# Performance work log

Measured on AMD Instinct MI355X. Metric: run time of the kernel, lower is better.

Reference implementation:

```python
import jax, jax.numpy as jnp
import numpy as np

N, IN_DIM, OUT_DIM, NUM_HOPS, SD = 8192, 256, 256, 4, 64
ETA, LAM_LAP, LAM_SP, EPS = 0.5, 0.3, 0.05, 0.5
LN_EPS = 1e-5


def setup_inputs() -> dict:
    key = jax.random.key(0)
    ks = jax.random.split(key, 6)
    K = NUM_HOPS + 1
    return {
        "H": jax.random.normal(ks[0], (N, IN_DIM), jnp.float32),
        "hops": jax.random.normal(ks[1], (K, N, IN_DIM), jnp.float32),
        "L": jax.random.normal(ks[2], (N, N), jnp.float32),
        "U": jax.random.normal(ks[3], (K, IN_DIM, SD), jnp.float32) * 0.1,
        "W_in": jax.random.normal(ks[4], (OUT_DIM, IN_DIM), jnp.float32) * 0.05,
        "ln_gamma": jnp.ones((OUT_DIM,), jnp.float32),
        "ln_beta": jnp.zeros((OUT_DIM,), jnp.float32),
        "log_tau": jnp.zeros((), jnp.float32),
    }


def _per_hop(U_k, H_k):
    n = H_k.shape[0]
    Q, _ = jnp.linalg.qr(U_k)                 # [in_dim, sd]
    Z = Q.T @ H_k.T                           # [sd, n]
    G = Z @ Z.T                               # [sd, sd] Gram, reused
    Sigma = G / (n + 1e-8)
    tr_S = jnp.trace(Sigma)
    tr_S2 = jnp.sum(Sigma * Sigma)            # trace(Sigma @ Sigma), Sigma symmetric
    rank_eff = tr_S ** 2 / (tr_S2 + 1e-8)
    coeff = SD / (n * EPS ** 2 + 1e-8)
    M = jnp.eye(SD, dtype=Z.dtype) + coeff * G
    Lc = jnp.linalg.cholesky(M)
    MiZ = jax.scipy.linalg.cho_solve((Lc, True), Z)  # [sd, n]
    grad_R = (Q @ MiZ).T                      # [n, in_dim]
    return rank_eff, grad_R


def reference(H, hops, L, U, W_in, ln_gamma, ln_beta, log_tau):
    tau = jnp.clip(jnp.exp(log_tau), 0.1, 10.0)
    rank_effs, grads_R = jax.vmap(_per_hop)(U, hops)      # [K], [K,n,in_dim]
    lap_terms = jnp.einsum('nm,kmd->knd', L, hops)        # [K,n,in_dim]
    w = jax.nn.softmax(rank_effs / tau)                   # [K]
    grad_sum = jnp.einsum('k,knd->nd', w, grads_R)
    lap_sum = jnp.einsum('k,knd->nd', w, lap_terms)
    H_half = H + ETA * grad_sum - ETA * LAM_LAP * lap_sum
    H_prox = jnp.sign(H_half) * jax.nn.relu(jnp.abs(H_half) - LAM_SP * ETA)
    H_out = H_prox @ W_in.T
    mu = jnp.mean(H_out, axis=-1, keepdims=True)
    var = jnp.var(H_out, axis=-1, keepdims=True)
    H_out = (H_out - mu) * jax.lax.rsqrt(var + LN_EPS) * ln_gamma + ln_beta
    return H_out, rank_effs, w
```

## Files before the change

### kernel.cpp

```cpp
#include <hip/hip_runtime.h>
#include <stdint.h>


typedef __attribute__((ext_vector_type(8))) short  s16x8;
typedef __attribute__((ext_vector_type(4))) float  f32x4;

#define NNODE 8192
#define DIN   256
#define KHOP  5
#define SDM   64

static const size_t OFF_Q    = 0;
static const size_t OFF_QT   = OFF_Q   + (size_t)5*256*64*4;
static const size_t OFF_ZT   = OFF_QT  + (size_t)5*64*256*2;
static const size_t OFF_GP   = OFF_ZT  + (size_t)5*8192*64*2;
static const size_t OFF_LM   = OFF_GP  + (size_t)5*16*4096*4;
static const size_t OFF_RD   = OFF_LM  + (size_t)5*4096*4;
static const size_t OFF_LU   = OFF_RD  + (size_t)5*64*4;
static const size_t OFF_RDU  = OFF_LU  + (size_t)5*4096*4;
static const size_t OFF_RE   = OFF_RDU + (size_t)5*64*4;
static const size_t OFF_W    = OFF_RE  + 64;
static const size_t OFF_T2   = OFF_W   + 64;
static const size_t OFF_HWT  = OFF_T2  + (size_t)5*256*64*2;
static const size_t OFF_WBF  = OFF_HWT + (size_t)256*8192*2;
static const size_t OFF_HP   = OFF_WBF + (size_t)256*256*2;
static const size_t OFF_PART = OFF_HP  + (size_t)8192*256*2;
static const size_t OFF_HPRE = OFF_PART;
static const size_t OFF_LBF  = OFF_PART + (size_t)9*8192*256*2;

__device__ __forceinline__ unsigned short f2bf(float f){
  unsigned u = __builtin_bit_cast(unsigned, f);
  u += 0x7FFFu + ((u >> 16) & 1u);
  return (unsigned short)(u >> 16);
}
__device__ __forceinline__ float bf2f(unsigned h){
  return __builtin_bit_cast(float, h << 16);
}
__device__ __forceinline__ void gl_lds16(const void* g, void* l){
  __builtin_amdgcn_global_load_lds(
      (const __attribute__((address_space(1))) void*)g,
      (__attribute__((address_space(3))) void*)l, 16, 0, 0);
}
__device__ __forceinline__ f32x4 mfma16(s16x8 a, s16x8 b, f32x4 c){
  return __builtin_amdgcn_mfma_f32_16x16x32_bf16(a, b, c, 0, 0, 0);
}

__device__ void chol64(float* A, float* rd, int tid){
  #pragma unroll 1
  for (int j = 0; j < 64; ++j){
    if (tid == 0){
      float d = sqrtf(fmaxf(A[j*65+j], 1e-20f));
      A[j*65+j] = d; rd[j] = 1.0f / d;
    }
    __syncthreads();
    float rinv = rd[j];
    for (int i = j+1+tid; i < 64; i += 256) A[i*65+j] *= rinv;
    __syncthreads();
    int rem = 63 - j;
    for (int e = tid; e < rem*rem; e += 256){
      int i = j+1 + e/rem;
      int l = j+1 + (e - (e/rem)*rem);
      if (l <= i) A[i*65+l] -= A[i*65+j] * A[l*65+j];
    }
    __syncthreads();
  }
}

__global__ __launch_bounds__(256) void k_lbf(const float* __restrict__ L,
                                             unsigned short* __restrict__ Lbf){
  size_t e = ((size_t)blockIdx.x*256 + threadIdx.x)*8;
  f32x4 a = *(const f32x4*)(L + e);
  f32x4 b = *(const f32x4*)(L + e + 4);
  uint4 u;
  u.x = (unsigned)f2bf(a[0]) | ((unsigned)f2bf(a[1]) << 16);
  u.y = (unsigned)f2bf(a[2]) | ((unsigned)f2bf(a[3]) << 16);
  u.z = (unsigned)f2bf(b[0]) | ((unsigned)f2bf(b[1]) << 16);
  u.w = (unsigned)f2bf(b[2]) | ((unsigned)f2bf(b[3]) << 16);
  *(uint4*)(Lbf + e) = u;
}

__global__ __launch_bounds__(256) void k_gramchol(const float* __restrict__ U,
                                                  float* __restrict__ Lu,
                                                  float* __restrict__ rdu){
  int k = blockIdx.x, tid = threadIdx.x;
  __shared__ float Ul[256*65];
  __shared__ float A[64*65];
  __shared__ float rd[64];
  const float* Uk = U + (size_t)k*16384;
  for (int e = tid; e < 16384; e += 256) Ul[(e>>6)*65 + (e&63)] = Uk[e];
  __syncthreads();
  int ti = tid >> 4, tj = tid & 15;
  float s[16];
  #pragma unroll
  for (int i = 0; i < 16; ++i) s[i] = 0.0f;
  for (int n = 0; n < 256; ++n){
    float xa[4], xb[4];
    #pragma unroll
    for (int p = 0; p < 4; ++p){ xa[p] = Ul[n*65 + ti*4 + p]; xb[p] = Ul[n*65 + tj*4 + p]; }
    #pragma unroll
    for (int p = 0; p < 4; ++p)
      #pragma unroll
      for (int q = 0; q < 4; ++q) s[p*4+q] += xa[p]*xb[q];
  }
  #pragma unroll
  for (int p = 0; p < 4; ++p)
    #pragma unroll
    for (int q = 0; q < 4; ++q) A[(ti*4+p)*65 + tj*4+q] = s[p*4+q];
  __syncthreads();
  chol64(A, rd, tid);
  for (int e = tid; e < 4096; e += 256) Lu[(size_t)k*4096 + e] = A[(e>>6)*65 + (e&63)];
  if (tid < 64) rdu[k*64 + tid] = rd[tid];
}

__global__ __launch_bounds__(256) void k_qsolve(const float* __restrict__ U,
                                                const float* __restrict__ Lu,
                                                const float* __restrict__ rdu,
                                                float* __restrict__ Qf,
                                                unsigned short* __restrict__ Qt){
  int k = blockIdx.y, tid = threadIdx.x, wave = tid >> 6, lane = tid & 63;
  __shared__ float Al[64*65];
  __shared__ float rds[64];
  for (int e = tid; e < 4096; e += 256) Al[(e>>6)*65 + (e&63)] = Lu[(size_t)k*4096 + e];
  if (tid < 64) rds[tid] = rdu[k*64 + tid];
  __syncthreads();
  int n = blockIdx.x*4 + wave;
  float x = U[((size_t)k*256 + n)*64 + lane];
  #pragma unroll
  for (int j = 0; j < 64; ++j){
    float zj = __shfl(x, j) * rds[j];
    x = (lane == j) ? zj : (lane > j ? x - Al[lane*65+j]*zj : x);
  }
  Qf[((size_t)k*256 + n)*64 + lane] = x;
  Qt[(size_t)k*16384 + lane*256 + n] = f2bf(x);
}

__global__ __launch_bounds__(256,2) void k_zgemm(const float* __restrict__ hops,
                                                 const unsigned short* __restrict__ Qt,
                                                 unsigned short* __restrict__ Zt){
  __shared__ __align__(16) unsigned short Al[128][72];
  __shared__ __align__(16) unsigned short Bl[64][64];
  int tid = threadIdx.x, lane = tid & 63, wave = tid >> 6;
  int q = lane >> 4, r = lane & 15;
  int k = blockIdx.y, m0 = blockIdx.x * 128;
  f32x4 acc[2][4];
  #pragma unroll
  for (int a = 0; a < 2; ++a)
    #pragma unroll
    for (int b = 0; b < 4; ++b) acc[a][b] = (f32x4){0,0,0,0};
  int rr = tid >> 1, half = tid & 1;
  for (int it = 0; it < 4; ++it){
    __syncthreads();
    #pragma unroll
    for (int i = 0; i < 2; ++i){
      int o = i*4096 + wave*1024 + lane*16;
      int srow = o >> 7, kc = (o & 127) >> 1;
      gl_lds16(Qt + (size_t)k*16384 + srow*256 + it*64 + kc,
               (char*)&Bl[0][0] + i*4096 + wave*1024);
    }
    const float* ga = hops + ((size_t)k*NNODE + m0 + rr)*256 + it*64 + half*32;
    f32x4 v[8];
    #pragma unroll
    for (int i = 0; i < 8; ++i) v[i] = *(const f32x4*)(ga + i*4);
    #pragma unroll
    for (int i = 0; i < 4; ++i){
      s16x8 t;
      #pragma unroll
      for (int j = 0; j < 8; ++j){ int e = i*8+j; t[j] = (short)f2bf(v[e>>2][e&3]); }
      *(s16x8*)&Al[rr][half*32 + i*8] = t;
    }
    __syncthreads();
    #pragma unroll
    for (int h = 0; h < 2; ++h){
      int ko = h*32 + q*8;
      s16x8 b[4];
      #pragma unroll
      for (int ni = 0; ni < 4; ++ni) b[ni] = *(const s16x8*)&Bl[ni*16 + r][ko];
      #pragma unroll
      for (int mi = 0; mi < 2; ++mi){
        s16x8 a = *(const s16x8*)&Al[wave*32 + mi*16 + r][ko];
        #pragma unroll
        for (int ni = 0; ni < 4; ++ni) acc[mi][ni] = mfma16(a, b[ni], acc[mi][ni]);
      }
    }
  }
  #pragma unroll
  for (int mi = 0; mi < 2; ++mi)
    #pragma unroll
    for (int ni = 0; ni < 4; ++ni)
      #pragma unroll
      for (int ii = 0; ii < 4; ++ii){
        int m = m0 + wave*32 + mi*16 + q*4 + ii;
        int sc = ni*16 + r;
        Zt[((size_t)k*NNODE + m)*64 + sc] = f2bf(acc[mi][ni][ii]);
      }
}

__global__ __launch_bounds__(256) void k_gpart(const unsigned short* __restrict__ Zt,
                                               float* __restrict__ Gp){
  int k = blockIdx.x, c = blockIdx.y, tid = threadIdx.x;
  __shared__ __align__(16) unsigned short Zl[128][64];
  int ti = tid >> 4, tj = tid & 15;
  float acc[16];
  #pragma unroll
  for (int i = 0; i < 16; ++i) acc[i] = 0.0f;
  for (int sub = 0; sub < 4; ++sub){
    const char* gb = (const char*)Zt + ((size_t)k*NNODE + c*512 + sub*128)*128;
    __syncthreads();
    #pragma unroll
    for (int i = 0; i < 4; ++i){
      int o = i*4096 + tid*16;
      *(uint4*)((char*)&Zl[0][0] + o) = *(const uint4*)(gb + o);
    }
    __syncthreads();
    for (int n = 0; n < 128; ++n){
      const unsigned short* row = &Zl[n][0];
      uint2 ua = *(const uint2*)(row + ti*4);
      uint2 ub = *(const uint2*)(row + tj*4);
      float xa[4] = { bf2f(ua.x & 0xffff), bf2f(ua.x >> 16), bf2f(ua.y & 0xffff), bf2f(ua.y >> 16) };
      float xb[4] = { bf2f(ub.x & 0xffff), bf2f(ub.x >> 16), bf2f(ub.y & 0xffff), bf2f(ub.y >> 16) };
      #pragma unroll
      for (int p = 0; p < 4; ++p)
        #pragma unroll
        for (int qn = 0; qn < 4; ++qn) acc[p*4+qn] += xa[p]*xb[qn];
    }
  }
  float* o = Gp + ((size_t)k*16 + c)*4096;
  #pragma unroll
  for (int p = 0; p < 4; ++p)
    #pragma unroll
    for (int qn = 0; qn < 4; ++qn) o[(ti*4+p)*64 + tj*4+qn] = acc[p*4+qn];
}

__global__ __launch_bounds__(256) void k_gred(const float* __restrict__ Gp,
                                              float* __restrict__ LmO,
                                              float* __restrict__ rdO,
                                              float* __restrict__ reO){
  int k = blockIdx.x, tid = threadIdx.x;
  __shared__ float A[64*65];
  __shared__ float rd[64];
  __shared__ float red[256];
  int ti = tid >> 4, tj = tid & 15;
  float s[16];
  #pragma unroll
  for (int i = 0; i < 16; ++i) s[i] = 0.0f;
  for (int c = 0; c < 16; ++c){
    const float* g = Gp + ((size_t)k*16 + c)*4096 + (ti*4)*64 + tj*4;
    #pragma unroll
    for (int p = 0; p < 4; ++p)
      #pragma unroll
      for (int qn = 0; qn < 4; ++qn) s[p*4+qn] += g[p*64+qn];
  }
  const float sc    = 1.0f / (8192.0f + 1e-8f);
  const float coeff = 64.0f / (8192.0f*0.25f + 1e-8f);
  float trp = 0.0f, tr2p = 0.0f;
  #pragma unroll
  for (int p = 0; p < 4; ++p)
    #pragma unroll
    for (int qn = 0; qn < 4; ++qn){
      float gg = s[p*4+qn];
      float sg = gg * sc;
      tr2p += sg*sg;
      int row = ti*4+p, col = tj*4+qn;
      if (row == col) trp += sg;
      A[row*65 + col] = (row == col ? 1.0f : 0.0f) + coeff*gg;
    }
  red[tid] = trp; __syncthreads();
  for (int o = 128; o > 0; o >>= 1){ if (tid < o) red[tid] += red[tid+o]; __syncthreads(); }
  float tr = red[0]; __syncthreads();
  red[tid] = tr2p; __syncthreads();
  for (int o = 128; o > 0; o >>= 1){ if (tid < o) red[tid] += red[tid+o]; __syncthreads(); }
  float tr2 = red[0]; __syncthreads();
  if (tid == 0) reO[k] = tr*tr / (tr2 + 1e-8f);
  chol64(A, rd, tid);
  for (int e = tid; e < 4096; e += 256) LmO[(size_t)k*4096 + e] = A[(e>>6)*65 + (e&63)];
  if (tid < 64) rdO[k*64 + tid] = rd[tid];
}

__global__ void k_soft(const float* __restrict__ re, const float* __restrict__ ltau,
                       float* __restrict__ wv, float* __restrict__ dtail){
  if (threadIdx.x == 0){
    float tau = expf(ltau[0]);
    tau = fminf(fmaxf(tau, 0.1f), 10.0f);
    float r[5], m = -1e30f;
    for (int i = 0; i < 5; ++i){ r[i] = re[i]; m = fmaxf(m, r[i]); }
    float e[5], sum = 0.0f;
    for (int i = 0; i < 5; ++i){ e[i] = expf((r[i]-m)/tau); sum += e[i]; }
    for (int i = 0; i < 5; ++i){
      float w = e[i]/sum;
      wv[i] = w; dtail[i] = r[i]; dtail[5+i] = w;
    }
  }
}

__global__ __launch_bounds__(256) void k_t2w(const float* __restrict__ Qf,
                                             const float* __restrict__ LmI,
                                             const float* __restrict__ rdI,
                                             const float* __restrict__ wv,
                                             unsigned short* __restrict__ T2w){
  int k = blockIdx.y, tid = threadIdx.x, wave = tid >> 6, lane = tid & 63;
  __shared__ float Al[64*65];
  __shared__ float rds[64];
  for (int e = tid; e < 4096; e += 256) Al[(e>>6)*65 + (e&63)] = LmI[(size_t)k*4096 + e];
  if (tid < 64) rds[tid] = rdI[k*64 + tid];
  __syncthreads();
  int n = blockIdx.x*4 + wave;
  float x = Qf[((size_t)k*256 + n)*64 + lane];
  #pragma unroll
  for (int j = 0; j < 64; ++j){
    float zj = __shfl(x, j) * rds[j];
    x = (lane == j) ? zj : (lane > j ? x - Al[lane*65+j]*zj : x);
  }
  #pragma unroll
  for (int j = 63; j >= 0; --j){
    float yj = __shfl(x, j) * rds[j];
    x = (lane == j) ? yj : (lane < j ? x - Al[j*65+lane]*yj : x);
  }
  float scale = 0.5f * wv[k];
  T2w[((size_t)k*256 + n)*64 + lane] = f2bf(scale * x);
}

__global__ __launch_bounds__(256) void k_hwT(const float* __restrict__ hops,
                                             const float* __restrict__ wv,
                                             unsigned short* __restrict__ hwT){
  __shared__ float T[64*65];
  int n0 = blockIdx.x*64, d0 = blockIdx.y*64, tid = threadIdx.x;
  float wl[5];
  #pragma unroll
  for (int k = 0; k < 5; ++k) wl[k] = -0.15f * wv[k];
  for (int e = tid; e < 1024; e += 256){
    int row = e >> 4, c4 = (e & 15)*4;
    f32x4 acc = (f32x4){0,0,0,0};
    #pragma unroll
    for (int k = 0; k < 5; ++k){
      f32x4 v = *(const f32x4*)(hops + ((size_t)k*NNODE + n0 + row)*256 + d0 + c4);
      acc += v * wl[k];
    }
    T[row*65 + c4+0] = acc[0]; T[row*65 + c4+1] = acc[1];
    T[row*65 + c4+2] = acc[2]; T[row*65 + c4+3] = acc[3];
  }
  __syncthreads();
  for (int e = tid; e < 1024; e += 256){
    int dr = e >> 4, c4 = (e & 15)*4;
    unsigned short h0 = f2bf(T[(c4+0)*65 + dr]);
    unsigned short h1 = f2bf(T[(c4+1)*65 + dr]);
    unsigned short h2 = f2bf(T[(c4+2)*65 + dr]);
    unsigned short h3 = f2bf(T[(c4+3)*65 + dr]);
    uint2 u; u.x = (unsigned)h0 | ((unsigned)h1 << 16); u.y = (unsigned)h2 | ((unsigned)h3 << 16);
    *(uint2*)(hwT + (size_t)(d0+dr)*NNODE + n0 + c4) = u;
  }
}

__global__ void k_wbf(const float* __restrict__ W, unsigned short* __restrict__ Wbf){
  int e = (blockIdx.x*256 + threadIdx.x)*4;
  f32x4 v = *(const f32x4*)(W + e);
  uint2 u;
  u.x = (unsigned)f2bf(v[0]) | ((unsigned)f2bf(v[1]) << 16);
  u.y = (unsigned)f2bf(v[2]) | ((unsigned)f2bf(v[3]) << 16);
  *(uint2*)(Wbf + e) = u;
}

__global__ __launch_bounds__(256,2) void k_biggemm(const unsigned short* __restrict__ Lbf,
                                                   const unsigned short* __restrict__ Bt,
                                                   unsigned short* __restrict__ part){
  __shared__ __align__(16) unsigned short Al[16*520];
  __shared__ __align__(16) unsigned short Bl[32*520];
  int tid = threadIdx.x, lane = tid & 63, wave = tid >> 6;
  int q = lane >> 4, r = lane & 15;
  int m0 = blockIdx.x * 128;
  size_t kbase = (size_t)blockIdx.y * 1024;
  int sr = lane >> 3, sc8 = (lane & 7) * 8;
  f32x4 acc[8][4];
  #pragma unroll
  for (int a = 0; a < 8; ++a)
    #pragma unroll
    for (int b = 0; b < 4; ++b) acc[a][b] = (f32x4){0,0,0,0};
  for (int it = 0; it < 16; ++it){
    size_t k0 = kbase + it*64;
    __syncthreads();
    #pragma unroll
    for (int i = 0; i < 12; ++i){
      int c = i*4 + wave;
      if (c < 16){
        gl_lds16(Lbf + (size_t)(m0 + c*8 + sr)*NNODE + k0 + sc8,
                 (char*)Al + c*1040 + lane*16);
      } else {
        int cb = c - 16;
        gl_lds16(Bt + (size_t)(cb*8 + sr)*NNODE + k0 + sc8,
                 (char*)Bl + cb*1040 + lane*16);
      }
    }
    __syncthreads();
    #pragma unroll
    for (int h = 0; h < 2; ++h){
      int ko = h*32 + q*8;
      s16x8 b[4];
      #pragma unroll
      for (int ni = 0; ni < 4; ++ni){
        int d = wave*64 + ni*16 + r;
        b[ni] = *(const s16x8*)(Bl + (d>>3)*520 + (d&7)*64 + ko);
      }
      #pragma unroll
      for (int mi = 0; mi < 8; ++mi){
        int m = mi*16 + r;
        s16x8 a = *(const s16x8*)(Al + (m>>3)*520 + (m&7)*64 + ko);
        #pragma unroll
        for (int ni = 0; ni < 4; ++ni) acc[mi][ni] = mfma16(a, b[ni], acc[mi][ni]);
      }
    }
  }
  unsigned short* o = part + (size_t)blockIdx.y * 2097152;
  #pragma unroll
  for (int mi = 0; mi < 8; ++mi)
    #pragma unroll
    for (int ni = 0; ni < 4; ++ni)
      #pragma unroll
      for (int ii = 0; ii < 4; ++ii){
        int m = m0 + mi*16 + q*4 + ii;
        int n = wave*64 + ni*16 + r;
        o[(size_t)m*256 + n] = f2bf(acc[mi][ni][ii]);
      }
}

__global__ __launch_bounds__(256,2) void k_gradgemm(const unsigned short* __restrict__ Zt,
                                                    const unsigned short* __restrict__ T2w,
                                                    unsigned short* __restrict__ out){
  __shared__ __align__(16) unsigned short Al[32][64];
  __shared__ __align__(16) unsigned short Bl[256][64];
  int tid = threadIdx.x, lane = tid & 63, wave = tid >> 6;
  int q = lane >> 4, r = lane & 15;
  int m0 = blockIdx.x * 32;
  f32x4 acc[2][4];
  #pragma unroll
  for (int a = 0; a < 2; ++a)
    #pragma unroll
    for (int b = 0; b < 4; ++b) acc[a][b] = (f32x4){0,0,0,0};
  for (int kk = 0; kk < 5; ++kk){
    __syncthreads();
    {
      int o = wave*1024 + lane*16;
      gl_lds16((const char*)Zt + ((size_t)kk*NNODE + m0)*128 + o,
               (char*)&Al[0][0] + wave*1024);
    }
    #pragma unroll
    for (int i = 0; i < 8; ++i){
      int o = i*4096 + wave*1024 + lane*16;
      gl_lds16((const char*)T2w + (size_t)kk*32768 + o,
               (char*)&Bl[0][0] + i*4096 + wave*1024);
    }
    __syncthreads();
    #pragma unroll
    for (int h = 0; h < 2; ++h){
      int ko = h*32 + q*8;
      s16x8 b[4];
      #pragma unroll
      for (int ni = 0; ni < 4; ++ni) b[ni] = *(const s16x8*)&Bl[wave*64 + ni*16 + r][ko];
      #pragma unroll
      for (int mi = 0; mi < 2; ++mi){
        s16x8 a = *(const s16x8*)&Al[mi*16 + r][ko];
        #pragma unroll
        for (int ni = 0; ni < 4; ++ni) acc[mi][ni] = mfma16(a, b[ni], acc[mi][ni]);
      }
    }
  }
  #pragma unroll
  for (int mi = 0; mi < 2; ++mi)
    #pragma unroll
    for (int ni = 0; ni < 4; ++ni)
      #pragma unroll
      for (int ii = 0; ii < 4; ++ii){
        int m = m0 + mi*16 + q*4 + ii;
        int n = wave*64 + ni*16 + r;
        out[(size_t)m*256 + n] = f2bf(acc[mi][ni][ii]);
      }
}

__global__ __launch_bounds__(256) void k_combine(const float* __restrict__ H,
                                                 const unsigned short* __restrict__ part,
                                                 unsigned short* __restrict__ Hp){
  size_t e = ((size_t)blockIdx.x*256 + threadIdx.x)*4;
  f32x4 h = *(const f32x4*)(H + e);
  float s0 = h[0], s1 = h[1], s2 = h[2], s3 = h[3];
  #pragma unroll
  for (int sl = 0; sl < 9; ++sl){
    uint2 u = *(const uint2*)(part + (size_t)sl*2097152 + e);
    s0 += bf2f(u.x & 0xffff); s1 += bf2f(u.x >> 16);
    s2 += bf2f(u.y & 0xffff); s3 += bf2f(u.y >> 16);
  }
  #define PROX(a) ({ float _t = fabsf(a) - 0.025f; _t > 0.0f ? copysignf(_t,(a)) : 0.0f; })
  uint2 o;
  o.x = (unsigned)f2bf(PROX(s0)) | ((unsigned)f2bf(PROX(s1)) << 16);
  o.y = (unsigned)f2bf(PROX(s2)) | ((unsigned)f2bf(PROX(s3)) << 16);
  *(uint2*)(Hp + e) = o;
}

__global__ __launch_bounds__(256,2) void k_fingemm(const unsigned short* __restrict__ Hp,
                                                   const unsigned short* __restrict__ Wbf,
                                                   float* __restrict__ Hpre){
  __shared__ __align__(16) unsigned short Al[64][64];
  __shared__ __align__(16) unsigned short Bl[256][64];
  int tid = threadIdx.x, lane = tid & 63, wave = tid >> 6;
  int q = lane >> 4, r = lane & 15;
  int m0 = blockIdx.x * 64;
  f32x4 acc[4][4];
  #pragma unroll
  for (int a = 0; a < 4; ++a)
    #pragma unroll
    for (int b = 0; b < 4; ++b) acc[a][b] = (f32x4){0,0,0,0};
  for (int it = 0; it < 4; ++it){
    __syncthreads();
    #pragma unroll
    for (int i = 0; i < 2; ++i){
      int o = i*4096 + wave*1024 + lane*16;
      int row = o >> 7, kc = o & 127;
      gl_lds16((const char*)Hp + (size_t)(m0+row)*512 + it*128 + kc,
               (char*)&Al[0][0] + i*4096 + wave*1024);
    }
    #pragma unroll
    for (int i = 0; i < 8; ++i){
      int o = i*4096 + wave*1024 + lane*16;
      int n = o >> 7, kc = o & 127;
      gl_lds16((const char*)Wbf + (size_t)n*512 + it*128 + kc,
               (char*)&Bl[0][0] + i*4096 + wave*1024);
    }
    __syncthreads();
    #pragma unroll
    for (int h = 0; h < 2; ++h){
      int ko = h*32 + q*8;
      s16x8 b[4];
      #pragma unroll
      for (int ni = 0; ni < 4; ++ni) b[ni] = *(const s16x8*)&Bl[wave*64 + ni*16 + r][ko];
      #pragma unroll
      for (int mi = 0; mi < 4; ++mi){
        s16x8 a = *(const s16x8*)&Al[mi*16 + r][ko];
        #pragma unroll
        for (int ni = 0; ni < 4; ++ni) acc[mi][ni] = mfma16(a, b[ni], acc[mi][ni]);
      }
    }
  }
  #pragma unroll
  for (int mi = 0; mi < 4; ++mi)
    #pragma unroll
    for (int ni = 0; ni < 4; ++ni)
      #pragma unroll
      for (int ii = 0; ii < 4; ++ii){
        int m = m0 + mi*16 + q*4 + ii;
        int n = wave*64 + ni*16 + r;
        Hpre[(size_t)m*256 + n] = acc[mi][ni][ii];
      }
}

__global__ __launch_bounds__(256) void k_ln(const float* __restrict__ Hpre,
                                            const float* __restrict__ gamma,
                                            const float* __restrict__ beta,
                                            float* __restrict__ out){
  int row = blockIdx.x*4 + (threadIdx.x >> 6);
  int lane = threadIdx.x & 63;
  f32x4 x = *(const f32x4*)(Hpre + (size_t)row*256 + lane*4);
  float sm = x[0]+x[1]+x[2]+x[3];
  float sq = x[0]*x[0]+x[1]*x[1]+x[2]*x[2]+x[3]*x[3];
  #pragma unroll
  for (int o = 1; o < 64; o <<= 1){ sm += __shfl_xor(sm, o, 64); sq += __shfl_xor(sq, o, 64); }
  float mean = sm * (1.0f/256.0f);
  float var  = sq * (1.0f/256.0f) - mean*mean;
  float rs   = rsqrtf(var + 1e-5f);
  f32x4 g = *(const f32x4*)(gamma + lane*4);
  f32x4 b = *(const f32x4*)(beta  + lane*4);
  f32x4 y;
  #pragma unroll
  for (int i = 0; i < 4; ++i) y[i] = (x[i]-mean)*rs*g[i] + b[i];
  *(f32x4*)(out + (size_t)row*256 + lane*4) = y;
}

extern "C" void kernel_launch(void* const* d_in, const int* in_sizes, int n_in,
                              void* d_out, int out_size, void* d_ws, size_t ws_size,
                              hipStream_t stream){
  const float* H    = (const float*)d_in[0];
  const float* hops = (const float*)d_in[1];
  const float* Lmat = (const float*)d_in[2];
  const float* U    = (const float*)d_in[3];
  const float* Win  = (const float*)d_in[4];
  const float* gam  = (const float*)d_in[5];
  const float* bet  = (const float*)d_in[6];
  const float* ltau = (const float*)d_in[7];
  float* out = (float*)d_out;

  char* ws = (char*)d_ws;
  float*          Qf   = (float*)(ws + OFF_Q);
  unsigned short* Qt   = (unsigned short*)(ws + OFF_QT);
  unsigned short* Zt   = (unsigned short*)(ws + OFF_ZT);
  float*          Gp   = (float*)(ws + OFF_GP);
  float*          Lm   = (float*)(ws + OFF_LM);
  float*          rdw  = (float*)(ws + OFF_RD);
  float*          Lu   = (float*)(ws + OFF_LU);
  float*          rdu  = (float*)(ws + OFF_RDU);
  float*          re   = (float*)(ws + OFF_RE);
  float*          wv   = (float*)(ws + OFF_W);
  unsigned short* T2w  = (unsigned short*)(ws + OFF_T2);
  unsigned short* hwT  = (unsigned short*)(ws + OFF_HWT);
  unsigned short* Wbf  = (unsigned short*)(ws + OFF_WBF);
  unsigned short* Hp   = (unsigned short*)(ws + OFF_HP);
  unsigned short* part = (unsigned short*)(ws + OFF_PART);
  float*          Hpre = (float*)(ws + OFF_HPRE);
  unsigned short* Lbf  = (unsigned short*)(ws + OFF_LBF);

  hipLaunchKernelGGL(k_lbf,     dim3(32768),    dim3(256), 0, stream, Lmat, Lbf);
  hipLaunchKernelGGL(k_gramchol,dim3(5),        dim3(256), 0, stream, U, Lu, rdu);
  hipLaunchKernelGGL(k_qsolve,  dim3(64,5),     dim3(256), 0, stream, U, Lu, rdu, Qf, Qt);
  hipLaunchKernelGGL(k_zgemm,   dim3(64,5),     dim3(256), 0, stream, hops, Qt, Zt);
  hipLaunchKernelGGL(k_gpart,   dim3(5,16),     dim3(256), 0, stream, Zt, Gp);
  hipLaunchKernelGGL(k_gred,    dim3(5),        dim3(256), 0, stream, Gp, Lm, rdw, re);
  hipLaunchKernelGGL(k_soft,    dim3(1),        dim3(64),  0, stream, re, ltau, wv, out + 2097152);
  hipLaunchKernelGGL(k_t2w,     dim3(64,5),     dim3(256), 0, stream, Qf, Lm, rdw, wv, T2w);
  hipLaunchKernelGGL(k_hwT,     dim3(128,4),    dim3(256), 0, stream, hops, wv, hwT);
  hipLaunchKernelGGL(k_wbf,     dim3(64),       dim3(256), 0, stream, Win, Wbf);
  hipLaunchKernelGGL(k_biggemm, dim3(64,8),     dim3(256), 0, stream, Lbf, hwT, part);
  hipLaunchKernelGGL(k_gradgemm,dim3(256),      dim3(256), 0, stream, Zt, T2w, part + (size_t)8*2097152);
  hipLaunchKernelGGL(k_combine, dim3(2048),     dim3(256), 0, stream, H, part, Hp);
  hipLaunchKernelGGL(k_fingemm, dim3(128),      dim3(256), 0, stream, Hp, Wbf, Hpre);
  hipLaunchKernelGGL(k_ln,      dim3(2048),     dim3(256), 0, stream, Hpre, gam, bet, out);
}
```

Before: 730.3 us.

## Merge independent launches into combined kernels and fuse LayerNorm into final GEMM

Combines the L bf16 conversion with the U Gram-Cholesky into one launch, and merges hwT, T2w and Wbf preparation into one kernel by block index. Also merges the big Laplacian GEMM and the grad GEMM into one grid. LayerNorm is fused into the final GEMM epilogue through an LDS row reduction, so the fp32 Hpre round trip goes away. The Cholesky update loop is simplified to a flat 4096-element sweep, and the Gram step reads U straight from global memory instead of staging it in LDS. The aims are fewer launches, overlap of small independent work, and less memory traffic, at the cost of heterogeneous blocks sharing one LDS and register budget.

Measured after the change: 752.9 us. 1.03x slower.

```diff
diff --git a/kernel.cpp b/kernel.cpp
--- a/kernel.cpp
+++ b/kernel.cpp
@@ -25,7 +25,6 @@
 static const size_t OFF_WBF  = OFF_HWT + (size_t)256*8192*2;
 static const size_t OFF_HP   = OFF_WBF + (size_t)256*256*2;
 static const size_t OFF_PART = OFF_HP  + (size_t)8192*256*2;
-static const size_t OFF_HPRE = OFF_PART;
 static const size_t OFF_LBF  = OFF_PART + (size_t)9*8192*256*2;
 
 __device__ __forceinline__ unsigned short f2bf(float f){
@@ -56,47 +55,44 @@
     float rinv = rd[j];
     for (int i = j+1+tid; i < 64; i += 256) A[i*65+j] *= rinv;
     __syncthreads();
-    int rem = 63 - j;
-    for (int e = tid; e < rem*rem; e += 256){
-      int i = j+1 + e/rem;
-      int l = j+1 + (e - (e/rem)*rem);
-      if (l <= i) A[i*65+l] -= A[i*65+j] * A[l*65+j];
-    }
-    __syncthreads();
-  }
-}
-
-__global__ __launch_bounds__(256) void k_lbf(const float* __restrict__ L,
+    #pragma unroll 1
+    for (int e = tid; e < 4096; e += 256){
+      int i = e >> 6, l = e & 63;
+      if (i > j && l > j && l <= i) A[i*65+l] -= A[i*65+j] * A[l*65+j];
+    }
+    __syncthreads();
+  }
+}
+
+__global__ __launch_bounds__(256) void k_pre(const float* __restrict__ U,
+                                             const float* __restrict__ L,
+                                             float* __restrict__ Lu,
+                                             float* __restrict__ rdu,
                                              unsigned short* __restrict__ Lbf){
-  size_t e = ((size_t)blockIdx.x*256 + threadIdx.x)*8;
-  f32x4 a = *(const f32x4*)(L + e);
-  f32x4 b = *(const f32x4*)(L + e + 4);
-  uint4 u;
-  u.x = (unsigned)f2bf(a[0]) | ((unsigned)f2bf(a[1]) << 16);
-  u.y = (unsigned)f2bf(a[2]) | ((unsigned)f2bf(a[3]) << 16);
-  u.z = (unsigned)f2bf(b[0]) | ((unsigned)f2bf(b[1]) << 16);
-  u.w = (unsigned)f2bf(b[2]) | ((unsigned)f2bf(b[3]) << 16);
-  *(uint4*)(Lbf + e) = u;
-}
-
-__global__ __launch_bounds__(256) void k_gramchol(const float* __restrict__ U,
-                                                  float* __restrict__ Lu,
-                                                  float* __restrict__ rdu){
-  int k = blockIdx.x, tid = threadIdx.x;
-  __shared__ float Ul[256*65];
   __shared__ float A[64*65];
   __shared__ float rd[64];
+  int tid = threadIdx.x;
+  if (blockIdx.x >= 5){
+    size_t e = ((size_t)(blockIdx.x-5)*256 + tid)*8;
+    f32x4 a = *(const f32x4*)(L + e);
+    f32x4 b = *(const f32x4*)(L + e + 4);
+    uint4 u;
+    u.x = (unsigned)f2bf(a[0]) | ((unsigned)f2bf(a[1]) << 16);
+    u.y = (unsigned)f2bf(a[2]) | ((unsigned)f2bf(a[3]) << 16);
+    u.z = (unsigned)f2bf(b[0]) | ((unsigned)f2bf(b[1]) << 16);
+    u.w = (unsigned)f2bf(b[2]) | ((unsigned)f2bf(b[3]) << 16);
+    *(uint4*)(Lbf + e) = u;
+    return;
+  }
+  int k = blockIdx.x;
   const float* Uk = U + (size_t)k*16384;
-  for (int e = tid; e < 16384; e += 256) Ul[(e>>6)*65 + (e&63)] = Uk[e];
-  __syncthreads();
   int ti = tid >> 4, tj = tid & 15;
   float s[16];
   #pragma unroll
   for (int i = 0; i < 16; ++i) s[i] = 0.0f;
   for (int n = 0; n < 256; ++n){
-    float xa[4], xb[4];
-    #pragma unroll
-    for (int p = 0; p < 4; ++p){ xa[p] = Ul[n*65 + ti*4 + p]; xb[p] = Ul[n*65 + tj*4 + p]; }
+    f32x4 xa = *(const f32x4*)(Uk + n*64 + ti*4);
+    f32x4 xb = *(const f32x4*)(Uk + n*64 + tj*4);
     #pragma unroll
     for (int p = 0; p < 4; ++p)
       #pragma unroll
@@ -292,186 +288,191 @@
   }
 }
 
-__global__ __launch_bounds__(256) void k_t2w(const float* __restrict__ Qf,
-                                             const float* __restrict__ LmI,
-                                             const float* __restrict__ rdI,
-                                             const float* __restrict__ wv,
-                                             unsigned short* __restrict__ T2w){
-  int k = blockIdx.y, tid = threadIdx.x, wave = tid >> 6, lane = tid & 63;
-  __shared__ float Al[64*65];
+__global__ __launch_bounds__(256) void k_post(const float* __restrict__ hops,
+                                              const float* __restrict__ wv,
+                                              unsigned short* __restrict__ hwT,
+                                              const float* __restrict__ Qf,
+                                              const float* __restrict__ LmI,
+                                              const float* __restrict__ rdI,
+                                              unsigned short* __restrict__ T2w,
+                                              const float* __restrict__ Win,
+                                              unsigned short* __restrict__ Wbf){
+  __shared__ float T[64*65];
   __shared__ float rds[64];
-  for (int e = tid; e < 4096; e += 256) Al[(e>>6)*65 + (e&63)] = LmI[(size_t)k*4096 + e];
-  if (tid < 64) rds[tid] = rdI[k*64 + tid];
-  __syncthreads();
-  int n = blockIdx.x*4 + wave;
-  float x = Qf[((size_t)k*256 + n)*64 + lane];
-  #pragma unroll
-  for (int j = 0; j < 64; ++j){
-    float zj = __shfl(x, j) * rds[j];
-    x = (lane == j) ? zj : (lane > j ? x - Al[lane*65+j]*zj : x);
-  }
-  #pragma unroll
-  for (int j = 63; j >= 0; --j){
-    float yj = __shfl(x, j) * rds[j];
-    x = (lane == j) ? yj : (lane < j ? x - Al[j*65+lane]*yj : x);
-  }
-  float scale = 0.5f * wv[k];
-  T2w[((size_t)k*256 + n)*64 + lane] = f2bf(scale * x);
-}
-
-__global__ __launch_bounds__(256) void k_hwT(const float* __restrict__ hops,
-                                             const float* __restrict__ wv,
-                                             unsigned short* __restrict__ hwT){
-  __shared__ float T[64*65];
-  int n0 = blockIdx.x*64, d0 = blockIdx.y*64, tid = threadIdx.x;
-  float wl[5];
-  #pragma unroll
-  for (int k = 0; k < 5; ++k) wl[k] = -0.15f * wv[k];
-  for (int e = tid; e < 1024; e += 256){
-    int row = e >> 4, c4 = (e & 15)*4;
-    f32x4 acc = (f32x4){0,0,0,0};
-    #pragma unroll
-    for (int k = 0; k < 5; ++k){
-      f32x4 v = *(const f32x4*)(hops + ((size_t)k*NNODE + n0 + row)*256 + d0 + c4);
-      acc += v * wl[k];
-    }
-    T[row*65 + c4+0] = acc[0]; T[row*65 + c4+1] = acc[1];
-    T[row*65 + c4+2] = acc[2]; T[row*65 + c4+3] = acc[3];
-  }
-  __syncthreads();
-  for (int e = tid; e < 1024; e += 256){
-    int dr = e >> 4, c4 = (e & 15)*4;
-    unsigned short h0 = f2bf(T[(c4+0)*65 + dr]);
-    unsigned short h1 = f2bf(T[(c4+1)*65 + dr]);
-    unsigned short h2 = f2bf(T[(c4+2)*65 + dr]);
-    unsigned short h3 = f2bf(T[(c4+3)*65 + dr]);
-    uint2 u; u.x = (unsigned)h0 | ((unsigned)h1 << 16); u.y = (unsigned)h2 | ((unsigned)h3 << 16);
-    *(uint2*)(hwT + (size_t)(d0+dr)*NNODE + n0 + c4) = u;
-  }
-}
-
-__global__ void k_wbf(const float* __restrict__ W, unsigned short* __restrict__ Wbf){
-  int e = (blockIdx.x*256 + threadIdx.x)*4;
-  f32x4 v = *(const f32x4*)(W + e);
-  uint2 u;
-  u.x = (unsigned)f2bf(v[0]) | ((unsigned)f2bf(v[1]) << 16);
-  u.y = (unsigned)f2bf(v[2]) | ((unsigned)f2bf(v[3]) << 16);
-  *(uint2*)(Wbf + e) = u;
-}
-
-__global__ __launch_bounds__(256,2) void k_biggemm(const unsigned short* __restrict__ Lbf,
-                                                   const unsigned short* __restrict__ Bt,
-                                                   unsigned short* __restrict__ part){
-  __shared__ __align__(16) unsigned short Al[16*520];
-  __shared__ __align__(16) unsigned short Bl[32*520];
-  int tid = threadIdx.x, lane = tid & 63, wave = tid >> 6;
+  int bid = blockIdx.x, tid = threadIdx.x;
+  if (bid < 512){
+    int n0 = (bid & 127)*64, d0 = (bid >> 7)*64;
+    float wl[5];
+    #pragma unroll
+    for (int k = 0; k < 5; ++k) wl[k] = -0.15f * wv[k];
+    for (int e = tid; e < 1024; e += 256){
+      int row = e >> 4, c4 = (e & 15)*4;
+      f32x4 acc = (f32x4){0,0,0,0};
+      #pragma unroll
+      for (int k = 0; k < 5; ++k){
+        f32x4 v = *(const f32x4*)(hops + ((size_t)k*NNODE + n0 + row)*256 + d0 + c4);
+        acc += v * wl[k];
+      }
+      T[row*65 + c4+0] = acc[0]; T[row*65 + c4+1] = acc[1];
+      T[row*65 + c4+2] = acc[2]; T[row*65 + c4+3] = acc[3];
+    }
+    __syncthreads();
+    for (int e = tid; e < 1024; e += 256){
+      int dr = e >> 4, c4 = (e & 15)*4;
+      unsigned short h0 = f2bf(T[(c4+0)*65 + dr]);
+      unsigned short h1 = f2bf(T[(c4+1)*65 + dr]);
+      unsigned short h2 = f2bf(T[(c4+2)*65 + dr]);
+      unsigned short h3 = f2bf(T[(c4+3)*65 + dr]);
+      uint2 u; u.x = (unsigned)h0 | ((unsigned)h1 << 16); u.y = (unsigned)h2 | ((unsigned)h3 << 16);
+      *(uint2*)(hwT + (size_t)(d0+dr)*NNODE + n0 + c4) = u;
+    }
+  } else if (bid < 832){
+    int i = bid - 512;
+    int k = i >> 6, xb = i & 63;
+    int wave = tid >> 6, lane = tid & 63;
+    for (int e = tid; e < 4096; e += 256) T[(e>>6)*65 + (e&63)] = LmI[(size_t)k*4096 + e];
+    if (tid < 64) rds[tid] = rdI[k*64 + tid];
+    __syncthreads();
+    int n = xb*4 + wave;
+    float x = Qf[((size_t)k*256 + n)*64 + lane];
+    #pragma unroll
+    for (int j = 0; j < 64; ++j){
+      float zj = __shfl(x, j) * rds[j];
+      x = (lane == j) ? zj : (lane > j ? x - T[lane*65+j]*zj : x);
+    }
+    #pragma unroll
+    for (int j = 63; j >= 0; --j){
+      float yj = __shfl(x, j) * rds[j];
+      x = (lane == j) ? yj : (lane < j ? x - T[j*65+lane]*yj : x);
+    }
+    float scale = 0.5f * wv[k];
+    T2w[((size_t)k*256 + n)*64 + lane] = f2bf(scale * x);
+  } else {
+    int i = bid - 832;
+    int e = (i*256 + tid)*4;
+    f32x4 v = *(const f32x4*)(Win + e);
+    uint2 u;
+    u.x = (unsigned)f2bf(v[0]) | ((unsigned)f2bf(v[1]) << 16);
+    u.y = (unsigned)f2bf(v[2]) | ((unsigned)f2bf(v[3]) << 16);
+    *(uint2*)(Wbf + e) = u;
+  }
+}
+
+__global__ __launch_bounds__(256,2) void k_gg(const unsigned short* __restrict__ Lbf,
+                                              const unsigned short* __restrict__ Bt,
+                                              unsigned short* __restrict__ part,
+                                              const unsigned short* __restrict__ Zt,
+                                              const unsigned short* __restrict__ T2w){
+  __shared__ __align__(16) unsigned short SM[24960];
+  int bid = blockIdx.x, tid = threadIdx.x;
+  int lane = tid & 63, wave = tid >> 6;
   int q = lane >> 4, r = lane & 15;
-  int m0 = blockIdx.x * 128;
-  size_t kbase = (size_t)blockIdx.y * 1024;
-  int sr = lane >> 3, sc8 = (lane & 7) * 8;
-  f32x4 acc[8][4];
-  #pragma unroll
-  for (int a = 0; a < 8; ++a)
-    #pragma unroll
-    for (int b = 0; b < 4; ++b) acc[a][b] = (f32x4){0,0,0,0};
-  for (int it = 0; it < 16; ++it){
-    size_t k0 = kbase + it*64;
-    __syncthreads();
-    #pragma unroll
-    for (int i = 0; i < 12; ++i){
-      int c = i*4 + wave;
-      if (c < 16){
-        gl_lds16(Lbf + (size_t)(m0 + c*8 + sr)*NNODE + k0 + sc8,
-                 (char*)Al + c*1040 + lane*16);
-      } else {
-        int cb = c - 16;
-        gl_lds16(Bt + (size_t)(cb*8 + sr)*NNODE + k0 + sc8,
-                 (char*)Bl + cb*1040 + lane*16);
-      }
-    }
-    __syncthreads();
-    #pragma unroll
-    for (int h = 0; h < 2; ++h){
-      int ko = h*32 + q*8;
-      s16x8 b[4];
-      #pragma unroll
-      for (int ni = 0; ni < 4; ++ni){
-        int d = wave*64 + ni*16 + r;
-        b[ni] = *(const s16x8*)(Bl + (d>>3)*520 + (d&7)*64 + ko);
-      }
-      #pragma unroll
-      for (int mi = 0; mi < 8; ++mi){
-        int m = mi*16 + r;
-        s16x8 a = *(const s16x8*)(Al + (m>>3)*520 + (m&7)*64 + ko);
-        #pragma unroll
-        for (int ni = 0; ni < 4; ++ni) acc[mi][ni] = mfma16(a, b[ni], acc[mi][ni]);
-      }
-    }
-  }
-  unsigned short* o = part + (size_t)blockIdx.y * 2097152;
-  #pragma unroll
-  for (int mi = 0; mi < 8; ++mi)
-    #pragma unroll
-    for (int ni = 0; ni < 4; ++ni)
-      #pragma unroll
-      for (int ii = 0; ii < 4; ++ii){
-        int m = m0 + mi*16 + q*4 + ii;
-        int n = wave*64 + ni*16 + r;
-        o[(size_t)m*256 + n] = f2bf(acc[mi][ni][ii]);
-      }
-}
-
-__global__ __launch_bounds__(256,2) void k_gradgemm(const unsigned short* __restrict__ Zt,
-                                                    const unsigned short* __restrict__ T2w,
-                                                    unsigned short* __restrict__ out){
-  __shared__ __align__(16) unsigned short Al[32][64];
-  __shared__ __align__(16) unsigned short Bl[256][64];
-  int tid = threadIdx.x, lane = tid & 63, wave = tid >> 6;
-  int q = lane >> 4, r = lane & 15;
-  int m0 = blockIdx.x * 32;
-  f32x4 acc[2][4];
-  #pragma unroll
-  for (int a = 0; a < 2; ++a)
-    #pragma unroll
-    for (int b = 0; b < 4; ++b) acc[a][b] = (f32x4){0,0,0,0};
-  for (int kk = 0; kk < 5; ++kk){
-    __syncthreads();
-    {
-      int o = wave*1024 + lane*16;
-      gl_lds16((const char*)Zt + ((size_t)kk*NNODE + m0)*128 + o,
-               (char*)&Al[0][0] + wave*1024);
-    }
-    #pragma unroll
-    for (int i = 0; i < 8; ++i){
-      int o = i*4096 + wave*1024 + lane*16;
-      gl_lds16((const char*)T2w + (size_t)kk*32768 + o,
-               (char*)&Bl[0][0] + i*4096 + wave*1024);
-    }
-    __syncthreads();
-    #pragma unroll
-    for (int h = 0; h < 2; ++h){
-      int ko = h*32 + q*8;
-      s16x8 b[4];
-      #pragma unroll
-      for (int ni = 0; ni < 4; ++ni) b[ni] = *(const s16x8*)&Bl[wave*64 + ni*16 + r][ko];
-      #pragma unroll
-      for (int mi = 0; mi < 2; ++mi){
-        s16x8 a = *(const s16x8*)&Al[mi*16 + r][ko];
-        #pragma unroll
-        for (int ni = 0; ni < 4; ++ni) acc[mi][ni] = mfma16(a, b[ni], acc[mi][ni]);
-      }
-    }
-  }
-  #pragma unroll
-  for (int mi = 0; mi < 2; ++mi)
-    #pragma unroll
-    for (int ni = 0; ni < 4; ++ni)
-      #pragma unroll
-      for (int ii = 0; ii < 4; ++ii){
-        int m = m0 + mi*16 + q*4 + ii;
-        int n = wave*64 + ni*16 + r;
-        out[(size_t)m*256 + n] = f2bf(acc[mi][ni][ii]);
-      }
+  if (bid < 512){
+    unsigned short* Al = SM;
+    unsigned short* Bl = SM + 16*520;
+    int m0 = (bid & 63) * 128;
+    int by = bid >> 6;
+    size_t kbase = (size_t)by * 1024;
+    int sr = lane >> 3, sc8 = (lane & 7) * 8;
+    f32x4 acc[8][4];
+    #pragma unroll
+    for (int a = 0; a < 8; ++a)
+      #pragma unroll
+      for (int b = 0; b < 4; ++b) acc[a][b] = (f32x4){0,0,0,0};
+    for (int it = 0; it < 16; ++it){
+      size_t k0 = kbase + it*64;
+      __syncthreads();
+      #pragma unroll
+      for (int i = 0; i < 12; ++i){
+        int c = i*4 + wave;
+        if (c < 16){
+          gl_lds16(Lbf + (size_t)(m0 + c*8 + sr)*NNODE + k0 + sc8,
+                   (char*)Al + c*1040 + lane*16);
+        } else {
+          int cb = c - 16;
+          gl_lds16(Bt + (size_t)(cb*8 + sr)*NNODE + k0 + sc8,
+                   (char*)Bl + cb*1040 + lane*16);
+        }
+      }
+      __syncthreads();
+      #pragma unroll
+      for (int h = 0; h < 2; ++h){
+        int ko = h*32 + q*8;
+        s16x8 b[4];
+        #pragma unroll
+        for (int ni = 0; ni < 4; ++ni){
+          int d = wave*64 + ni*16 + r;
+          b[ni] = *(const s16x8*)(Bl + (d>>3)*520 + (d&7)*64 + ko);
+        }
+        #pragma unroll
+        for (int mi = 0; mi < 8; ++mi){
+          int m = mi*16 + r;
+          s16x8 a = *(const s16x8*)(Al + (m>>3)*520 + (m&7)*64 + ko);
+          #pragma unroll
+          for (int ni = 0; ni < 4; ++ni) acc[mi][ni] = mfma16(a, b[ni], acc[mi][ni]);
+        }
+      }
+    }
+    unsigned short* o = part + (size_t)by * 2097152;
+    #pragma unroll
+    for (int mi = 0; mi < 8; ++mi)
+      #pragma unroll
+      for (int ni = 0; ni < 4; ++ni)
+        #pragma unroll
+        for (int ii = 0; ii < 4; ++ii){
+          int m = m0 + mi*16 + q*4 + ii;
+          int n = wave*64 + ni*16 + r;
+          o[(size_t)m*256 + n] = f2bf(acc[mi][ni][ii]);
+        }
+  } else {
+    unsigned short* Al = SM;
+    unsigned short* Bl = SM + 2048;
+    int m0 = (bid - 512) * 32;
+    f32x4 acc[2][4];
+    #pragma unroll
+    for (int a = 0; a < 2; ++a)
+      #pragma unroll
+      for (int b = 0; b < 4; ++b) acc[a][b] = (f32x4){0,0,0,0};
+    for (int kk = 0; kk < 5; ++kk){
+      __syncthreads();
+      {
+        int o = wave*1024 + lane*16;
+        gl_lds16((const char*)Zt + ((size_t)kk*NNODE + m0)*128 + o,
+                 (char*)Al + wave*1024);
+      }
+      #pragma unroll
+      for (int i = 0; i < 8; ++i){
+        int o = i*4096 + wave*1024 + lane*16;
+        gl_lds16((const char*)T2w + (size_t)kk*32768 + o,
+                 (char*)Bl + i*4096 + wave*1024);
+      }
+      __syncthreads();
+      #pragma unroll
+      for (int h = 0; h < 2; ++h){
+        int ko = h*32 + q*8;
+        s16x8 b[4];
+        #pragma unroll
+        for (int ni = 0; ni < 4; ++ni) b[ni] = *(const s16x8*)&Bl[(wave*64 + ni*16 + r)*64 + ko];
+        #pragma unroll
+        for (int mi = 0; mi < 2; ++mi){
+          s16x8 a = *(const s16x8*)&Al[(mi*16 + r)*64 + ko];
+          #pragma unroll
+          for (int ni = 0; ni < 4; ++ni) acc[mi][ni] = mfma16(a, b[ni], acc[mi][ni]);
+        }
+      }
+    }
+    unsigned short* o8 = part + (size_t)8 * 2097152;
+    #pragma unroll
+    for (int mi = 0; mi < 2; ++mi)
+      #pragma unroll
+      for (int ni = 0; ni < 4; ++ni)
+        #pragma unroll
+        for (int ii = 0; ii < 4; ++ii){
+          int m = m0 + mi*16 + q*4 + ii;
+          int n = wave*64 + ni*16 + r;
+          o8[(size_t)m*256 + n] = f2bf(acc[mi][ni][ii]);
+        }
+  }
 }
 
 __global__ __launch_bounds__(256) void k_combine(const float* __restrict__ H,
@@ -493,11 +494,15 @@
   *(uint2*)(Hp + e) = o;
 }
 
-__global__ __launch_bounds__(256,2) void k_fingemm(const unsigned short* __restrict__ Hp,
-                                                   const unsigned short* __restrict__ Wbf,
-                                                   float* __restrict__ Hpre){
+__global__ __launch_bounds__(256,2) void k_finln(const unsigned short* __restrict__ Hp,
+                                                 const unsigned short* __restrict__ Wbf,
+                                                 const float* __restrict__ gamma,
+                                                 const float* __restrict__ beta,
+                                                 float* __restrict__ out){
   __shared__ __align__(16) unsigned short Al[64][64];
   __shared__ __align__(16) unsigned short Bl[256][64];
+  __shared__ float SmR[64][4];
+  __shared__ float SqR[64][4];
   int tid = threadIdx.x, lane = tid & 63, wave = tid >> 6;
   int q = lane >> 4, r = lane & 15;
   int m0 = blockIdx.x * 64;
@@ -540,35 +545,43 @@
   #pragma unroll
   for (int mi = 0; mi < 4; ++mi)
     #pragma unroll
-    for (int ni = 0; ni < 4; ++ni)
-      #pragma unroll
-      for (int ii = 0; ii < 4; ++ii){
-        int m = m0 + mi*16 + q*4 + ii;
-        int n = wave*64 + ni*16 + r;
-        Hpre[(size_t)m*256 + n] = acc[mi][ni][ii];
-      }
-}
-
-__global__ __launch_bounds__(256) void k_ln(const float* __restrict__ Hpre,
-                                            const float* __restrict__ gamma,
-                                            const float* __restrict__ beta,
-                                            float* __restrict__ out){
-  int row = blockIdx.x*4 + (threadIdx.x >> 6);
-  int lane = threadIdx.x & 63;
-  f32x4 x = *(const f32x4*)(Hpre + (size_t)row*256 + lane*4);
-  float sm = x[0]+x[1]+x[2]+x[3];
-  float sq = x[0]*x[0]+x[1]*x[1]+x[2]*x[2]+x[3]*x[3];
-  #pragma unroll
-  for (int o = 1; o < 64; o <<= 1){ sm += __shfl_xor(sm, o, 64); sq += __shfl_xor(sq, o, 64); }
-  float mean = sm * (1.0f/256.0f);
-  float var  = sq * (1.0f/256.0f) - mean*mean;
-  float rs   = rsqrtf(var + 1e-5f);
-  f32x4 g = *(const f32x4*)(gamma + lane*4);
-  f32x4 b = *(const f32x4*)(beta  + lane*4);
-  f32x4 y;
-  #pragma unroll
-  for (int i = 0; i < 4; ++i) y[i] = (x[i]-mean)*rs*g[i] + b[i];
-  *(f32x4*)(out + (size_t)row*256 + lane*4) = y;
+    for (int ii = 0; ii < 4; ++ii){
+      float sm = 0.0f, sq = 0.0f;
+      #pragma unroll
+      for (int ni = 0; ni < 4; ++ni){
+        float v = acc[mi][ni][ii];
+        sm += v; sq += v*v;
+      }
+      #pragma unroll
+      for (int o = 1; o < 16; o <<= 1){ sm += __shfl_xor(sm, o, 64); sq += __shfl_xor(sq, o, 64); }
+      if (r == 0){
+        int rl = mi*16 + q*4 + ii;
+        SmR[rl][wave] = sm; SqR[rl][wave] = sq;
+      }
+    }
+  __syncthreads();
+  float g[4], b[4];
+  #pragma unroll
+  for (int ni = 0; ni < 4; ++ni){
+    g[ni] = gamma[wave*64 + ni*16 + r];
+    b[ni] = beta [wave*64 + ni*16 + r];
+  }
+  #pragma unroll
+  for (int mi = 0; mi < 4; ++mi)
+    #pragma unroll
+    for (int ii = 0; ii < 4; ++ii){
+      int rl = mi*16 + q*4 + ii;
+      float sm = SmR[rl][0] + SmR[rl][1] + SmR[rl][2] + SmR[rl][3];
+      float sq = SqR[rl][0] + SqR[rl][1] + SqR[rl][2] + SqR[rl][3];
+      float mean = sm * (1.0f/256.0f);
+      float var  = sq * (1.0f/256.0f) - mean*mean;
+      float rs   = rsqrtf(var + 1e-5f);
+      #pragma unroll
+      for (int ni = 0; ni < 4; ++ni){
+        out[(size_t)(m0+rl)*256 + wave*64 + ni*16 + r] =
+            (acc[mi][ni][ii] - mean)*rs*g[ni] + b[ni];
+      }
+    }
 }
 
 extern "C" void kernel_launch(void* const* d_in, const int* in_sizes, int n_in,
@@ -600,22 +613,16 @@
   unsigned short* Wbf  = (unsigned short*)(ws + OFF_WBF);
   unsigned short* Hp   = (unsigned short*)(ws + OFF_HP);
   unsigned short* part = (unsigned short*)(ws + OFF_PART);
-  float*          Hpre = (float*)(ws + OFF_HPRE);
   unsigned short* Lbf  = (unsigned short*)(ws + OFF_LBF);
 
-  hipLaunchKernelGGL(k_lbf,     dim3(32768),    dim3(256), 0, stream, Lmat, Lbf);
-  hipLaunchKernelGGL(k_gramchol,dim3(5),        dim3(256), 0, stream, U, Lu, rdu);
-  hipLaunchKernelGGL(k_qsolve,  dim3(64,5),     dim3(256), 0, stream, U, Lu, rdu, Qf, Qt);
-  hipLaunchKernelGGL(k_zgemm,   dim3(64,5),     dim3(256), 0, stream, hops, Qt, Zt);
-  hipLaunchKernelGGL(k_gpart,   dim3(5,16),     dim3(256), 0, stream, Zt, Gp);
-  hipLaunchKernelGGL(k_gred,    dim3(5),        dim3(256), 0, stream, Gp, Lm, rdw, re);
-  hipLaunchKernelGGL(k_soft,    dim3(1),        dim3(64),  0, stream, re, ltau, wv, out + 2097152);
-  hipLaunchKernelGGL(k_t2w,     dim3(64,5),     dim3(256), 0, stream, Qf, Lm, rdw, wv, T2w);
-  hipLaunchKernelGGL(k_hwT,     dim3(128,4),    dim3(256), 0, stream, hops, wv, hwT);
-  hipLaunchKernelGGL(k_wbf,     dim3(64),       dim3(256), 0, stream, Win, Wbf);
-  hipLaunchKernelGGL(k_biggemm, dim3(64,8),     dim3(256), 0, stream, Lbf, hwT, part);
-  hipLaunchKernelGGL(k_gradgemm,dim3(256),      dim3(256), 0, stream, Zt, T2w, part + (size_t)8*2097152);
-  hipLaunchKernelGGL(k_combine, dim3(2048),     dim3(256), 0, stream, H, part, Hp);
-  hipLaunchKernelGGL(k_fingemm, dim3(128),      dim3(256), 0, stream, Hp, Wbf, Hpre);
-  hipLaunchKernelGGL(k_ln,      dim3(2048),     dim3(256), 0, stream, Hpre, gam, bet, out);
-}
+  hipLaunchKernelGGL(k_pre,    dim3(32773),  dim3(256), 0, stream, U, Lmat, Lu, rdu, Lbf);
+  hipLaunchKernelGGL(k_qsolve, dim3(64,5),   dim3(256), 0, stream, U, Lu, rdu, Qf, Qt);
+  hipLaunchKernelGGL(k_zgemm,  dim3(64,5),   dim3(256), 0, stream, hops, Qt, Zt);
+  hipLaunchKernelGGL(k_gpart,  dim3(5,16),   dim3(256), 0, stream, Zt, Gp);
+  hipLaunchKernelGGL(k_gred,   dim3(5),      dim3(256), 0, stream, Gp, Lm, rdw, re);
+  hipLaunchKernelGGL(k_soft,   dim3(1),      dim3(64),  0, stream, re, ltau, wv, out + 2097152);
+  hipLaunchKernelGGL(k_post,   dim3(896),    dim3(256), 0, stream, hops, wv, hwT, Qf, Lm, rdw, T2w, Win, Wbf);
+  hipLaunchKernelGGL(k_gg,     dim3(768),    dim3(256), 0, stream, Lbf, hwT, part, Zt, T2w);
+  hipLaunchKernelGGL(k_combine,dim3(2048),   dim3(256), 0, stream, H, part, Hp);
+  hipLaunchKernelGGL(k_finln,  dim3(128),    dim3(256), 0, stream, Hp, Wbf, gam, bet, out);
+}
```
